# Optimization experiments

Hardware: AMD Instinct MI355X
Metric: run time of the kernel (lower is better)

## Reference

```python
import jax, jax.numpy as jnp
import numpy as np

NUM_HEADS = 8
WINDOW_SIZE = 4
DIM = 384


def setup_inputs() -> dict:
    key = jax.random.key(0)
    k_x, k_qkv, k_pw, k_pb = jax.random.split(key, 4)
    B, N, C = 8, 16384, DIM
    x = jax.random.normal(k_x, (B, N, C), dtype=jnp.float32)
    # torch nn.Linear weights are [out_features, in_features]
    W_qkv = jax.random.normal(k_qkv, (3 * C, C), dtype=jnp.float32) * (1.0 / np.sqrt(C))
    W_proj = jax.random.normal(k_pw, (C, C), dtype=jnp.float32) * (1.0 / np.sqrt(C))
    b_proj = jax.random.normal(k_pb, (C,), dtype=jnp.float32) * 0.01
    return {"x": x, "W_qkv": W_qkv, "W_proj": W_proj, "b_proj": b_proj}


def reference(x, W_qkv, W_proj, b_proj):
    B, N, C = x.shape
    H = int(round(N ** 0.5))
    W = H
    ws = WINDOW_SIZE
    nh = NUM_HEADS
    hd = C // nh
    scale = hd ** -0.5
    hw, ww = H // ws, W // ws

    qkv = x @ W_qkv.T  # [B, N, 3C]
    qkv = qkv.reshape(B, N, 3, nh, hd)
    qkv = jnp.transpose(qkv, (2, 0, 3, 1, 4))  # [3, B, nh, N, hd]
    q, k, v = qkv[0], qkv[1], qkv[2]

    def to_windows(t):
        # [B, nh, N, hd] -> [B, nh, n_windows, ws*ws, hd]
        t = t.reshape(B, nh, hw, ws, ww, ws, hd)
        t = jnp.transpose(t, (0, 1, 2, 4, 3, 5, 6))
        return t.reshape(B, nh, hw * ww, ws * ws, hd)

    q, k, v = to_windows(q), to_windows(k), to_windows(v)

    attn = jnp.einsum('bhwqd,bhwkd->bhwqk', q, k) * scale
    attn = jax.nn.softmax(attn, axis=-1)
    out = jnp.einsum('bhwqk,bhwkd->bhwqd', attn, v)

    # windows back to [B, N, C]
    out = out.reshape(B, nh, hw, ww, ws, ws, hd)
    out = jnp.transpose(out, (0, 1, 2, 4, 3, 5, 6)).reshape(B, nh, N, hd)
    out = jnp.transpose(out, (0, 2, 1, 3)).reshape(B, N, C)

    out = out @ W_proj.T + b_proj
    return out
```

## Files before the change

kernel.cpp:

```cpp
#include <hip/hip_runtime.h>
#include <hip/hip_bf16.h>
#include <cstdint>

#define ASPACE(n) __attribute__((address_space(n)))

typedef short bf16x8 __attribute__((ext_vector_type(8)));
typedef float f32x4 __attribute__((ext_vector_type(4)));

__device__ __forceinline__ unsigned short f2bf(float f) {
  uint32_t u = __float_as_uint(f);
  u += 0x7fffu + ((u >> 16) & 1u);
  return (unsigned short)(u >> 16);
}
__device__ __forceinline__ float bf2f(unsigned short h) {
  return __uint_as_float(((uint32_t)h) << 16);
}

__global__ __launch_bounds__(256) void conv_f32_bf16(const float4* __restrict__ src,
                                                     ushort4* __restrict__ dst, int n4) {
  int i = blockIdx.x * blockDim.x + threadIdx.x;
  int stride = gridDim.x * blockDim.x;
  for (; i < n4; i += stride) {
    float4 v = src[i];
    ushort4 o;
    o.x = f2bf(v.x); o.y = f2bf(v.y); o.z = f2bf(v.z); o.w = f2bf(v.w);
    dst[i] = o;
  }
}

__device__ __forceinline__ void gload16(const unsigned short* g, unsigned short* l) {
  __builtin_amdgcn_global_load_lds((const ASPACE(1) void*)g, (ASPACE(3) void*)l, 16, 0, 0);
}

__global__ __launch_bounds__(256, 3) void gemm_qkv(const unsigned short* __restrict__ A,
                                                   const unsigned short* __restrict__ B,
                                                   unsigned short* __restrict__ C,
                                                   int M, int N, int K) {
  __shared__ unsigned short As[2][128 * 32];
  __shared__ unsigned short Bs[2][192 * 32];

  const int tid  = threadIdx.x;
  const int lane = tid & 63;
  const int wave = tid >> 6;
  const int wr = wave >> 1;
  const int wc = wave & 1;

  const int nwg = gridDim.x;
  const int swz = (blockIdx.x & 7) * (nwg >> 3) + (blockIdx.x >> 3);
  const int ntn = N / 192;
  const int bn0 = (swz % ntn) * 192;
  const int bm0 = (swz / ntn) << 7;

  const unsigned short* Abase = A + (size_t)bm0 * K;
  const unsigned short* Bbase = B + (size_t)bn0 * K;

  const unsigned short* gA[2];
  const unsigned short* gB[3];
  unsigned short* lA[2];
  unsigned short* lB[3];
#pragma unroll
  for (int i = 0; i < 2; ++i) {
    const int c = i * 256 + tid;
    const int r = c >> 2;
    const int gc = (c & 3) ^ ((r >> 1) & 3);
    gA[i] = Abase + (size_t)r * K + gc * 8;
    lA[i] = (unsigned short*)As + (i * 256 + wave * 64) * 8;
  }
#pragma unroll
  for (int i = 0; i < 3; ++i) {
    const int c = i * 256 + tid;
    const int r = c >> 2;
    const int gc = (c & 3) ^ ((r >> 1) & 3);
    gB[i] = Bbase + (size_t)r * K + gc * 8;
    lB[i] = (unsigned short*)Bs + (i * 256 + wave * 64) * 8;
  }
  const int abufoff = 128 * 32;
  const int bbufoff = 192 * 32;

  const int fr = lane & 15;
  const int hi = lane >> 4;
  int afo[4], bfo[6];
#pragma unroll
  for (int m = 0; m < 4; ++m) {
    const int row = wr * 64 + m * 16 + fr;
    afo[m] = row * 32 + ((hi ^ ((row >> 1) & 3)) * 8);
  }
#pragma unroll
  for (int n = 0; n < 6; ++n) {
    const int row = wc * 96 + n * 16 + fr;
    bfo[n] = row * 32 + ((hi ^ ((row >> 1) & 3)) * 8);
  }

  f32x4 acc[4][6];
#pragma unroll
  for (int m = 0; m < 4; ++m)
#pragma unroll
    for (int n = 0; n < 6; ++n) {
      f32x4 z = {0.f, 0.f, 0.f, 0.f};
      acc[m][n] = z;
    }

  const int NT = K >> 5;

#pragma unroll
  for (int i = 0; i < 2; ++i) gload16(gA[i], lA[i]);
#pragma unroll
  for (int i = 0; i < 3; ++i) gload16(gB[i], lB[i]);
  __syncthreads();

  int cur = 0;
  for (int t = 0; t < NT; ++t) {
    if (t + 1 < NT) {
      const int nb = cur ^ 1;
      const int k0 = (t + 1) << 5;
#pragma unroll
      for (int i = 0; i < 2; ++i) gload16(gA[i] + k0, lA[i] + nb * abufoff);
#pragma unroll
      for (int i = 0; i < 3; ++i) gload16(gB[i] + k0, lB[i] + nb * bbufoff);
    }
    {
      const unsigned short* Ab = (const unsigned short*)As + cur * abufoff;
      const unsigned short* Bb = (const unsigned short*)Bs + cur * bbufoff;
      bf16x8 af[4], bfv[6];
#pragma unroll
      for (int m = 0; m < 4; ++m) af[m] = *(const bf16x8*)(Ab + afo[m]);
#pragma unroll
      for (int n = 0; n < 6; ++n) bfv[n] = *(const bf16x8*)(Bb + bfo[n]);
#pragma unroll
      for (int m = 0; m < 4; ++m)
#pragma unroll
        for (int n = 0; n < 6; ++n)
          acc[m][n] = __builtin_amdgcn_mfma_f32_16x16x32_bf16(af[m], bfv[n], acc[m][n], 0, 0, 0);
    }
    __syncthreads();
    cur ^= 1;
  }

  const int rq = hi * 4;
#pragma unroll
  for (int m = 0; m < 4; ++m) {
#pragma unroll
    for (int n = 0; n < 6; ++n) {
      const int col = bn0 + wc * 96 + n * 16 + fr;
      const int pl = col / 48;
      const int d  = col - pl * 48;
      unsigned short* base = C + ((size_t)pl * M + bm0 + wr * 64 + m * 16 + rq) * 48 + d;
#pragma unroll
      for (int r = 0; r < 4; ++r)
        base[(size_t)r * 48] = f2bf(acc[m][n][r]);
    }
  }
}

#define MTOK 131072
#define ASTR 392
__global__ __launch_bounds__(512, 2) void fused_attn_proj(const unsigned short* __restrict__ qkv,
                                                          const unsigned short* __restrict__ Wp,
                                                          const float* __restrict__ bias,
                                                          float* __restrict__ out) {
  __shared__ unsigned short lds[50176 + 24576];
  unsigned short* attn = lds;
  unsigned short* BsS  = lds + 50176;

  const int tid = threadIdx.x, lane = tid & 63, wave = tid >> 6;
  const int nwg = gridDim.x;
  const int swz = (blockIdx.x & 7) * (nwg >> 3) + (blockIdx.x >> 3);
  const int b = swz >> 7, g2 = swz & 127;
  const int yb = g2 >> 2, xb = g2 & 3;
  const int imgbase = b * 16384;

  const int lg = lane >> 4;
  const int lr = lane & 15;

  {
    unsigned short* Vt = BsS + wave * 1536;
    unsigned short* P  = Vt + 48 * 24;
    const int gtok = imgbase + (yb * 4 + (lr >> 2)) * 128 + xb * 32 + wave * 4 + (lr & 3);

    for (int h = 0; h < 8; ++h) {
      const size_t qb = ((size_t)h * MTOK + gtok) * 48;
      const size_t kb = ((size_t)(8 + h) * MTOK + gtok) * 48;
      const size_t vb = ((size_t)(16 + h) * MTOK + gtok) * 48;

      bf16x8 aq0 = *(const bf16x8*)(qkv + qb + lg * 8);
      bf16x8 bk0 = *(const bf16x8*)(qkv + kb + lg * 8);
      bf16x8 aq1 = {0, 0, 0, 0, 0, 0, 0, 0};
      bf16x8 bk1 = {0, 0, 0, 0, 0, 0, 0, 0};
      if (lg < 2) {
        aq1 = *(const bf16x8*)(qkv + qb + 32 + lg * 8);
        bk1 = *(const bf16x8*)(qkv + kb + 32 + lg * 8);
      }
      {
        bf16x8 v = *(const bf16x8*)(qkv + vb + lg * 8);
#pragma unroll
        for (int i = 0; i < 8; ++i) Vt[(lg * 8 + i) * 24 + lr] = (unsigned short)v[i];
        if (lane < 32) {
          bf16x8 v2 = *(const bf16x8*)(qkv + vb + 32 + lg * 8);
#pragma unroll
          for (int i = 0; i < 8; ++i) Vt[((4 + lg) * 8 + i) * 24 + lr] = (unsigned short)v2[i];
        }
      }

      f32x4 s = {0.f, 0.f, 0.f, 0.f};
      s = __builtin_amdgcn_mfma_f32_16x16x32_bf16(aq0, bk0, s, 0, 0, 0);
      s = __builtin_amdgcn_mfma_f32_16x16x32_bf16(aq1, bk1, s, 0, 0, 0);

      const float scale = 0.14433756729740643f;
      float p[4];
#pragma unroll
      for (int r = 0; r < 4; ++r) {
        float xv = s[r] * scale;
        float m = xv;
        m = fmaxf(m, __shfl_xor(m, 1));
        m = fmaxf(m, __shfl_xor(m, 2));
        m = fmaxf(m, __shfl_xor(m, 4));
        m = fmaxf(m, __shfl_xor(m, 8));
        float e = __expf(xv - m);
        float tt = e;
        tt += __shfl_xor(tt, 1);
        tt += __shfl_xor(tt, 2);
        tt += __shfl_xor(tt, 4);
        tt += __shfl_xor(tt, 8);
        p[r] = e / tt;
      }
#pragma unroll
      for (int r = 0; r < 4; ++r) P[(lg * 4 + r) * 24 + lr] = f2bf(p[r]);

      bf16x8 ap = {0, 0, 0, 0, 0, 0, 0, 0};
      if (lg < 2) ap = *(const bf16x8*)(P + lr * 24 + lg * 8);

      f32x4 o[3];
#pragma unroll
      for (int c = 0; c < 3; ++c) {
        bf16x8 bv = {0, 0, 0, 0, 0, 0, 0, 0};
        if (lg < 2) bv = *(const bf16x8*)(Vt + (c * 16 + lr) * 24 + lg * 8);
        f32x4 z = {0.f, 0.f, 0.f, 0.f};
        o[c] = __builtin_amdgcn_mfma_f32_16x16x32_bf16(ap, bv, z, 0, 0, 0);
      }

#pragma unroll
      for (int r = 0; r < 4; ++r) {
        const int qi = lg * 4 + r;
        const int lq = (qi >> 2) * 32 + wave * 4 + (qi & 3);
#pragma unroll
        for (int c = 0; c < 3; ++c)
          attn[lq * ASTR + h * 48 + c * 16 + lr] = f2bf(o[c][r]);
      }
    }
  }
  __syncthreads();

  const int fr = lane & 15;
  const int hi = lane >> 4;
  const int wr = wave >> 1;
  const int wc = wave & 1;

  const unsigned short* gB[3];
  unsigned short* lB[3];
#pragma unroll
  for (int i = 0; i < 3; ++i) {
    const int c = i * 512 + tid;
    const int r = c >> 2;
    const int gc = (c & 3) ^ ((r >> 1) & 3);
    gB[i] = Wp + (size_t)r * 384 + gc * 8;
    lB[i] = BsS + (i * 512 + wave * 64) * 8;
  }
  const int bbufoff = 384 * 32;

  int afo[2], bfo[12];
#pragma unroll
  for (int mf = 0; mf < 2; ++mf) {
    const int row = wr * 32 + mf * 16 + fr;
    afo[mf] = row * ASTR;
  }
#pragma unroll
  for (int nf = 0; nf < 12; ++nf) {
    const int row = wc * 192 + nf * 16 + fr;
    bfo[nf] = row * 32 + ((hi ^ ((row >> 1) & 3)) * 8);
  }

  f32x4 acc[2][12];
#pragma unroll
  for (int mf = 0; mf < 2; ++mf)
#pragma unroll
    for (int nf = 0; nf < 12; ++nf) {
      f32x4 z = {0.f, 0.f, 0.f, 0.f};
      acc[mf][nf] = z;
    }

#pragma unroll
  for (int i = 0; i < 3; ++i) gload16(gB[i], lB[i]);
  __syncthreads();

  int cur = 0;
  for (int t = 0; t < 12; ++t) {
    if (t + 1 < 12) {
      const int nb = cur ^ 1;
      const int k0 = (t + 1) << 5;
#pragma unroll
      for (int i = 0; i < 3; ++i) gload16(gB[i] + k0, lB[i] + nb * bbufoff);
    }
    {
      const unsigned short* Bb = BsS + cur * bbufoff;
      bf16x8 af[2], bfv[12];
#pragma unroll
      for (int mf = 0; mf < 2; ++mf)
        af[mf] = *(const bf16x8*)(attn + afo[mf] + t * 32 + hi * 8);
#pragma unroll
      for (int nf = 0; nf < 12; ++nf) bfv[nf] = *(const bf16x8*)(Bb + bfo[nf]);
#pragma unroll
      for (int mf = 0; mf < 2; ++mf)
#pragma unroll
        for (int nf = 0; nf < 12; ++nf)
          acc[mf][nf] = __builtin_amdgcn_mfma_f32_16x16x32_bf16(af[mf], bfv[nf], acc[mf][nf], 0, 0, 0);
    }
    __syncthreads();
    cur ^= 1;
  }

  const int rq = hi * 4;
#pragma unroll
  for (int mf = 0; mf < 2; ++mf) {
#pragma unroll
    for (int nf = 0; nf < 12; ++nf) {
      const int col = wc * 192 + nf * 16 + fr;
      const float bv = bias[col];
#pragma unroll
      for (int r = 0; r < 4; ++r) {
        const int l = wr * 32 + mf * 16 + rq + r;
        const int gtok = imgbase + (yb * 4 + (l >> 5)) * 128 + xb * 32 + (l & 31);
        out[(size_t)gtok * 384 + col] = acc[mf][nf][r] + bv;
      }
    }
  }
}

extern "C" void kernel_launch(void* const* d_in, const int* in_sizes, int n_in,
                              void* d_out, int out_size, void* d_ws, size_t ws_size,
                              hipStream_t stream) {
  const float* x      = (const float*)d_in[0];
  const float* W_qkv  = (const float*)d_in[1];
  const float* W_proj = (const float*)d_in[2];
  const float* b_proj = (const float*)d_in[3];
  float* out = (float*)d_out;

  const int Bb = 8, Nn = 16384, Cc = 384;
  const int M = Bb * Nn;
  const int threeC = 3 * Cc;

  char* ws = (char*)d_ws;
  unsigned short* qkv_bf   = (unsigned short*)ws;
  unsigned short* x_bf     = (unsigned short*)(ws + (size_t)M * threeC * 2);
  unsigned short* wqkv_bf  = (unsigned short*)(ws + (size_t)M * threeC * 2 + (size_t)M * Cc * 2);
  unsigned short* wproj_bf = wqkv_bf + threeC * Cc;

  conv_f32_bf16<<<2048, 256, 0, stream>>>((const float4*)x, (ushort4*)x_bf, M * Cc / 4);
  conv_f32_bf16<<<432, 256, 0, stream>>>((const float4*)W_qkv, (ushort4*)wqkv_bf, threeC * Cc / 4);
  conv_f32_bf16<<<144, 256, 0, stream>>>((const float4*)W_proj, (ushort4*)wproj_bf, Cc * Cc / 4);

  gemm_qkv<<<(M / 128) * (threeC / 192), 256, 0, stream>>>(x_bf, wqkv_bf, qkv_bf,
                                                           M, threeC, Cc);

  fused_attn_proj<<<M / 128, 512, 0, stream>>>(qkv_bf, wproj_bf, b_proj, out);
}
```

Before: 398.7 us.

## Fuse x fp32-to-bf16 conversion into QKV GEMM A-tile loads

Removes the separate conversion kernel for the activation tensor x. The QKV GEMM now loads fp32 x directly into registers, converts it with packed bf16 conversion instructions, and writes the result to the swizzled LDS buffer after the MFMA step. This avoids a full write and reread of a bf16 copy of x through global memory. In exchange, A-tile loads no longer go straight to LDS, so the GEMM reads twice as many bytes for A and spends more registers and VALU work per tile. Since each x tile is reread by all six N-tile blocks, that extra fp32 traffic is multiplied.

After: 387.1 us. 1.03x faster.

```diff
diff --git a/kernel.cpp b/kernel.cpp
--- a/kernel.cpp
+++ b/kernel.cpp
@@ -14,6 +14,15 @@
 }
 __device__ __forceinline__ float bf2f(unsigned short h) {
   return __uint_as_float(((uint32_t)h) << 16);
+}
+
+__device__ __forceinline__ bf16x8 cvt8(float4 a, float4 b) {
+  union { uint32_t u[4]; bf16x8 v; } r;
+  asm("v_cvt_pk_bf16_f32 %0, %1, %2" : "=v"(r.u[0]) : "v"(a.x), "v"(a.y));
+  asm("v_cvt_pk_bf16_f32 %0, %1, %2" : "=v"(r.u[1]) : "v"(a.z), "v"(a.w));
+  asm("v_cvt_pk_bf16_f32 %0, %1, %2" : "=v"(r.u[2]) : "v"(b.x), "v"(b.y));
+  asm("v_cvt_pk_bf16_f32 %0, %1, %2" : "=v"(r.u[3]) : "v"(b.z), "v"(b.w));
+  return r.v;
 }
 
 __global__ __launch_bounds__(256) void conv_f32_bf16(const float4* __restrict__ src,
@@ -32,7 +41,7 @@
   __builtin_amdgcn_global_load_lds((const ASPACE(1) void*)g, (ASPACE(3) void*)l, 16, 0, 0);
 }
 
-__global__ __launch_bounds__(256, 3) void gemm_qkv(const unsigned short* __restrict__ A,
+__global__ __launch_bounds__(256, 3) void gemm_qkv(const float* __restrict__ x,
                                                    const unsigned short* __restrict__ B,
                                                    unsigned short* __restrict__ C,
                                                    int M, int N, int K) {
@@ -51,21 +60,20 @@
   const int bn0 = (swz % ntn) * 192;
   const int bm0 = (swz / ntn) << 7;
 
-  const unsigned short* Abase = A + (size_t)bm0 * K;
   const unsigned short* Bbase = B + (size_t)bn0 * K;
 
-  const unsigned short* gA[2];
-  const unsigned short* gB[3];
-  unsigned short* lA[2];
-  unsigned short* lB[3];
+  const float* gAf[2];
+  int wAo[2];
 #pragma unroll
   for (int i = 0; i < 2; ++i) {
     const int c = i * 256 + tid;
     const int r = c >> 2;
     const int gc = (c & 3) ^ ((r >> 1) & 3);
-    gA[i] = Abase + (size_t)r * K + gc * 8;
-    lA[i] = (unsigned short*)As + (i * 256 + wave * 64) * 8;
-  }
+    gAf[i] = x + (size_t)(bm0 + r) * K + gc * 8;
+    wAo[i] = c * 8;
+  }
+  const unsigned short* gB[3];
+  unsigned short* lB[3];
 #pragma unroll
   for (int i = 0; i < 3; ++i) {
     const int c = i * 256 + tid;
@@ -102,19 +110,23 @@
 
   const int NT = K >> 5;
 
-#pragma unroll
-  for (int i = 0; i < 2; ++i) gload16(gA[i], lA[i]);
+  float4 a0[2], a1[2];
+#pragma unroll
+  for (int i = 0; i < 2; ++i) { a0[i] = *(const float4*)(gAf[i]); a1[i] = *(const float4*)(gAf[i] + 4); }
 #pragma unroll
   for (int i = 0; i < 3; ++i) gload16(gB[i], lB[i]);
+#pragma unroll
+  for (int i = 0; i < 2; ++i)
+    *(bf16x8*)((unsigned short*)As + wAo[i]) = cvt8(a0[i], a1[i]);
   __syncthreads();
 
   int cur = 0;
   for (int t = 0; t < NT; ++t) {
+    const int nb = cur ^ 1;
     if (t + 1 < NT) {
-      const int nb = cur ^ 1;
       const int k0 = (t + 1) << 5;
 #pragma unroll
-      for (int i = 0; i < 2; ++i) gload16(gA[i] + k0, lA[i] + nb * abufoff);
+      for (int i = 0; i < 2; ++i) { a0[i] = *(const float4*)(gAf[i] + k0); a1[i] = *(const float4*)(gAf[i] + k0 + 4); }
 #pragma unroll
       for (int i = 0; i < 3; ++i) gload16(gB[i] + k0, lB[i] + nb * bbufoff);
     }
@@ -131,6 +143,11 @@
 #pragma unroll
         for (int n = 0; n < 6; ++n)
           acc[m][n] = __builtin_amdgcn_mfma_f32_16x16x32_bf16(af[m], bfv[n], acc[m][n], 0, 0, 0);
+    }
+    if (t + 1 < NT) {
+#pragma unroll
+      for (int i = 0; i < 2; ++i)
+        *(bf16x8*)((unsigned short*)As + nb * abufoff + wAo[i]) = cvt8(a0[i], a1[i]);
     }
     __syncthreads();
     cur ^= 1;
@@ -350,15 +367,15 @@
 
   char* ws = (char*)d_ws;
   unsigned short* qkv_bf   = (unsigned short*)ws;
-  unsigned short* x_bf     = (unsigned short*)(ws + (size_t)M * threeC * 2);
-  unsigned short* wqkv_bf  = (unsigned short*)(ws + (size_t)M * threeC * 2 + (size_t)M * Cc * 2);
+  unsigned short* wqkv_bf  = (unsigned short*)(ws + (size_t)M * threeC * 2);
   unsigned short* wproj_bf = wqkv_bf + threeC * Cc;
 
-  conv_f32_bf16<<<2048, 256, 0, stream>>>((const float4*)x, (ushort4*)x_bf, M * Cc / 4);
-  conv_f32_bf16<<<432, 256, 0, stream>>>((const float4*)W_qkv, (ushort4*)wqkv_bf, threeC * Cc / 4);
-  conv_f32_bf16<<<144, 256, 0, stream>>>((const float4*)W_proj, (ushort4*)wproj_bf, Cc * Cc / 4);
-
-  gemm_qkv<<<(M / 128) * (threeC / 192), 256, 0, stream>>>(x_bf, wqkv_bf, qkv_bf,
+  conv_f32_bf16<<<432, 256, 0, stream>>>((const float4*)W_qkv, (ushort4*)wqkv_bf,
+                                         threeC * Cc / 4);
+  conv_f32_bf16<<<144, 256, 0, stream>>>((const float4*)W_proj, (ushort4*)wproj_bf,
+                                         Cc * Cc / 4);
+
+  gemm_qkv<<<(M / 128) * (threeC / 192), 256, 0, stream>>>(x, wqkv_bf, qkv_bf,
                                                            M, threeC, Cc);
 
   fused_attn_proj<<<M / 128, 512, 0, stream>>>(qkv_bf, wproj_bf, b_proj, out);
```
